# Kernel tuning notes

Hardware: AMD Instinct MI355X
Metric: run time of the kernel (lower is better)

Reference implementation:

```python
import jax, jax.numpy as jnp
import numpy as np

B, H, I = 64, 4096, 14336   # batch, hidden, expert intermediate
NLUT = 4096                 # 2**L_bits, L=12
W_SCALE = 0.02              # payload['W_scale'] (same for all three here)


def _rademacher(key, shape):
    return jnp.where(jax.random.bernoulli(key, 0.5, shape), 1.0, -1.0).astype(jnp.float32)


def setup_inputs() -> dict:
    key = jax.random.key(0)
    ks = jax.random.split(key, 14)
    inp = {
        "x": jax.random.normal(ks[0], (B, H), jnp.float32),
        "lut_gate": jax.random.normal(ks[1], (NLUT,), jnp.float32) * 0.05,
        "lut_up": jax.random.normal(ks[2], (NLUT,), jnp.float32) * 0.05,
        "lut_down": jax.random.normal(ks[3], (NLUT,), jnp.float32) * 0.05,
        "gate_walks": jax.random.randint(ks[4], (I, H), 0, NLUT, jnp.int32),
        "up_walks": jax.random.randint(ks[5], (I, H), 0, NLUT, jnp.int32),
        "down_walks": jax.random.randint(ks[6], (H, I), 0, NLUT, jnp.int32),
        "gate_sign_l": _rademacher(ks[7], (I,)),
        "gate_sign_r": _rademacher(ks[8], (H,)),
        "up_sign_l": _rademacher(ks[9], (I,)),
        "up_sign_r": _rademacher(ks[10], (H,)),
        "down_sign_l": _rademacher(ks[11], (H,)),
        "down_sign_r": _rademacher(ks[12], (I,)),
    }
    return inp


def _dequant(lut, walks, sign_l, sign_r):
    # trellis-walk LUT gather per weight element, then row/col signs and scalar scale
    # walks: (out, in) int codes; lut: (NLUT,)
    return (lut[walks] * sign_l[:, None] * sign_r[None, :]) * W_SCALE


def reference(x, lut_gate, lut_up, lut_down,
              gate_walks, up_walks, down_walks,
              gate_sign_l, gate_sign_r, up_sign_l, up_sign_r,
              down_sign_l, down_sign_r):
    W_gate = _dequant(lut_gate, gate_walks, gate_sign_l, gate_sign_r)  # (I, H)
    W_up = _dequant(lut_up, up_walks, up_sign_l, up_sign_r)            # (I, H)
    W_down = _dequant(lut_down, down_walks, down_sign_l, down_sign_r)  # (H, I)
    gate_out = jax.nn.silu(x @ W_gate.T)   # (B, I)
    up_out = x @ W_up.T                    # (B, I)
    hidden = gate_out * up_out
    return hidden @ W_down.T               # (B, H)
```

## Files before the change

kernel.cpp:

```cpp
#include <hip/hip_runtime.h>
#include <hip/hip_bf16.h>

#define HD   4096
#define ID   14336
#define NB   64
#define NLUTN 4096
#define DKS  8

typedef __attribute__((ext_vector_type(8))) short short8;
typedef __attribute__((ext_vector_type(4))) float f32x4;

__device__ __forceinline__ unsigned short f2bf(float f) {
  __hip_bfloat16 h = __float2bfloat16(f);
  return __builtin_bit_cast(unsigned short, h);
}

__device__ __forceinline__ void gll16(const int* g, void* l) {
  __builtin_amdgcn_global_load_lds(
      (const __attribute__((address_space(1))) int*)g,
      (__attribute__((address_space(3))) int*)l, 16, 0, 0);
}

__global__ __launch_bounds__(256) void prep_kernel(
    const float* __restrict__ x, const float* __restrict__ gsr,
    const float* __restrict__ usr,
    unsigned short* __restrict__ xgB, unsigned short* __restrict__ xuB)
{
  int u = blockIdx.x * 256 + threadIdx.x;
  int b = u & 63, k8 = u >> 6;
  const float* xp = x + (size_t)b * HD + k8 * 8;
  float4 x0 = ((const float4*)xp)[0];
  float4 x1 = ((const float4*)xp)[1];
  const float* gp = gsr + k8 * 8;
  const float* up = usr + k8 * 8;
  float4 g0 = ((const float4*)gp)[0], g1 = ((const float4*)gp)[1];
  float4 u0 = ((const float4*)up)[0], u1 = ((const float4*)up)[1];
  ushort4 og0 = make_ushort4(f2bf(x0.x*g0.x), f2bf(x0.y*g0.y), f2bf(x0.z*g0.z), f2bf(x0.w*g0.w));
  ushort4 og1 = make_ushort4(f2bf(x1.x*g1.x), f2bf(x1.y*g1.y), f2bf(x1.z*g1.z), f2bf(x1.w*g1.w));
  ushort4 ou0 = make_ushort4(f2bf(x0.x*u0.x), f2bf(x0.y*u0.y), f2bf(x0.z*u0.z), f2bf(x0.w*u0.w));
  ushort4 ou1 = make_ushort4(f2bf(x1.x*u1.x), f2bf(x1.y*u1.y), f2bf(x1.z*u1.z), f2bf(x1.w*u1.w));
  ((ushort4*)(xgB + (size_t)u*8))[0] = og0;
  ((ushort4*)(xgB + (size_t)u*8))[1] = og1;
  ((ushort4*)(xuB + (size_t)u*8))[0] = ou0;
  ((ushort4*)(xuB + (size_t)u*8))[1] = ou1;
}

__global__ __launch_bounds__(128, 2) void gate_up_kernel(
    const int* __restrict__ gw, const int* __restrict__ uw,
    const float* __restrict__ lutg_f, const float* __restrict__ lutu_f,
    const unsigned short* __restrict__ xgB, const unsigned short* __restrict__ xuB,
    const float* __restrict__ gsl, const float* __restrict__ usl,
    const float* __restrict__ dsr,
    unsigned short* __restrict__ hidB)
{
  __shared__ unsigned short lutg[NLUTN];
  __shared__ unsigned short lutu[NLUTN];
  __shared__ __align__(16) int cbuf[2][2][2][2][512];
  __shared__ f32x4 red[16][64];

  const int tid  = threadIdx.x;
  const int lane = tid & 63;
  const int w    = tid >> 6;

  for (int i = tid; i < NLUTN/4; i += 128) {
    float4 g = ((const float4*)lutg_f)[i];
    float4 u = ((const float4*)lutu_f)[i];
    ((ushort4*)lutg)[i] = make_ushort4(f2bf(g.x), f2bf(g.y), f2bf(g.z), f2bf(g.w));
    ((ushort4*)lutu)[i] = make_ushort4(f2bf(u.x), f2bf(u.y), f2bf(u.z), f2bf(u.w));
  }
  __syncthreads();

  const int col  = lane & 15;
  const int quad = lane >> 4;
  const int m0   = blockIdx.x * 32;
  const int r8   = lane >> 3;
  const int j    = lane & 7;
  const int jx   = (j ^ r8) << 2;
  const int xsw  = (col & 7) << 4;

  const int kbeg = w * (HD/2);
  const int NIT  = (HD/2) / 32;

  const int* gsrc[2][2];
  const int* usrc[2][2];
  #pragma unroll
  for (int s = 0; s < 2; ++s)
    #pragma unroll
    for (int h = 0; h < 2; ++h) {
      int row = m0 + s*16 + h*8 + r8;
      gsrc[s][h] = gw + (size_t)row * HD + jx;
      usrc[s][h] = uw + (size_t)row * HD + jx;
    }

  const f32x4 z = {0.f, 0.f, 0.f, 0.f};
  f32x4 accg[2][4] = {{z,z,z,z},{z,z,z,z}};
  f32x4 accu[2][4] = {{z,z,z,z},{z,z,z,z}};

  #pragma unroll
  for (int s = 0; s < 2; ++s)
    #pragma unroll
    for (int h = 0; h < 2; ++h) {
      gll16(gsrc[s][h] + kbeg, (char*)&cbuf[w][0][0][s][0] + h*1024);
      gll16(usrc[s][h] + kbeg, (char*)&cbuf[w][0][1][s][0] + h*1024);
    }

  int p = 0;
  for (int it = 0; it < NIT; ++it) {
    const int k0 = kbeg + it*32;
    asm volatile("s_waitcnt vmcnt(0)" ::: "memory");
    __builtin_amdgcn_sched_barrier(0);

    short8 afg[2], afu[2];
    #pragma unroll
    for (int s = 0; s < 2; ++s) {
      const char* cg = (const char*)&cbuf[w][p][0][s][0];
      const char* cu = (const char*)&cbuf[w][p][1][s][0];
      int4 ga = *(const int4*)(cg + col*128 + (((quad<<5) + 0 ) ^ xsw));
      int4 gb = *(const int4*)(cg + col*128 + (((quad<<5) + 16) ^ xsw));
      int4 ua = *(const int4*)(cu + col*128 + (((quad<<5) + 0 ) ^ xsw));
      int4 ub = *(const int4*)(cu + col*128 + (((quad<<5) + 16) ^ xsw));
      afg[s][0] = (short)lutg[ga.x]; afg[s][1] = (short)lutg[ga.y];
      afg[s][2] = (short)lutg[ga.z]; afg[s][3] = (short)lutg[ga.w];
      afg[s][4] = (short)lutg[gb.x]; afg[s][5] = (short)lutg[gb.y];
      afg[s][6] = (short)lutg[gb.z]; afg[s][7] = (short)lutg[gb.w];
      afu[s][0] = (short)lutu[ua.x]; afu[s][1] = (short)lutu[ua.y];
      afu[s][2] = (short)lutu[ua.z]; afu[s][3] = (short)lutu[ua.w];
      afu[s][4] = (short)lutu[ub.x]; afu[s][5] = (short)lutu[ub.y];
      afu[s][6] = (short)lutu[ub.z]; afu[s][7] = (short)lutu[ub.w];
    }

    const size_t xoff = ((size_t)((k0 >> 3) + quad) * 64 + col) * 8;
    short8 bgv[4], buv[4];
    #pragma unroll
    for (int t = 0; t < 4; ++t) {
      bgv[t] = __builtin_bit_cast(short8, *(const int4*)(xgB + xoff + t*128));
      buv[t] = __builtin_bit_cast(short8, *(const int4*)(xuB + xoff + t*128));
    }
    __builtin_amdgcn_sched_barrier(0);

    const int kn = (it == NIT-1) ? kbeg : k0 + 32;
    #pragma unroll
    for (int s = 0; s < 2; ++s)
      #pragma unroll
      for (int h = 0; h < 2; ++h) {
        gll16(gsrc[s][h] + kn, (char*)&cbuf[w][p^1][0][s][0] + h*1024);
        gll16(usrc[s][h] + kn, (char*)&cbuf[w][p^1][1][s][0] + h*1024);
      }

    #pragma unroll
    for (int t = 0; t < 4; ++t)
      #pragma unroll
      for (int s = 0; s < 2; ++s) {
        accg[s][t] = __builtin_amdgcn_mfma_f32_16x16x32_bf16(afg[s], bgv[t], accg[s][t], 0, 0, 0);
        accu[s][t] = __builtin_amdgcn_mfma_f32_16x16x32_bf16(afu[s], buv[t], accu[s][t], 0, 0, 0);
      }
    p ^= 1;
  }

  if (w == 1) {
    #pragma unroll
    for (int s = 0; s < 2; ++s)
      #pragma unroll
      for (int t = 0; t < 4; ++t) {
        red[(s*4+t)*2+0][lane] = accg[s][t];
        red[(s*4+t)*2+1][lane] = accu[s][t];
      }
  }
  __syncthreads();
  if (w == 0) {
    #pragma unroll
    for (int s = 0; s < 2; ++s) {
      const int mrow = m0 + s*16 + quad*4;
      float sg[4], su[4], sd[4];
      #pragma unroll
      for (int r = 0; r < 4; ++r) {
        sg[r] = 0.02f * gsl[mrow + r];
        su[r] = 0.02f * usl[mrow + r];
        sd[r] = dsr[mrow + r];
      }
      #pragma unroll
      for (int t = 0; t < 4; ++t) {
        f32x4 ag = accg[s][t] + red[(s*4+t)*2+0][lane];
        f32x4 au = accu[s][t] + red[(s*4+t)*2+1][lane];
        int b = t*16 + col;
        float g0 = ag[0]*sg[0], u0 = au[0]*su[0];
        float g1 = ag[1]*sg[1], u1 = au[1]*su[1];
        float g2 = ag[2]*sg[2], u2 = au[2]*su[2];
        float g3 = ag[3]*sg[3], u3 = au[3]*su[3];
        ushort4 hv;
        hv.x = f2bf((g0 / (1.f + __expf(-g0))) * u0 * sd[0]);
        hv.y = f2bf((g1 / (1.f + __expf(-g1))) * u1 * sd[1]);
        hv.z = f2bf((g2 / (1.f + __expf(-g2))) * u2 * sd[2]);
        hv.w = f2bf((g3 / (1.f + __expf(-g3))) * u3 * sd[3]);
        *(ushort4*)(hidB + ((size_t)((mrow >> 3)*64 + b))*8 + (quad & 1)*4) = hv;
      }
    }
  }
}

__global__ __launch_bounds__(128, 2) void down_kernel(
    const int* __restrict__ dw, const float* __restrict__ lutd_f,
    const unsigned short* __restrict__ hidB,
    const float* __restrict__ dsl,
    float* __restrict__ out)
{
  __shared__ unsigned short lutd[NLUTN];
  __shared__ __align__(16) int cbuf[2][2][2][512];
  __shared__ f32x4 red[8][64];

  const int tid  = threadIdx.x;
  const int lane = tid & 63;
  const int w    = tid >> 6;

  for (int i = tid; i < NLUTN/4; i += 128) {
    float4 d = ((const float4*)lutd_f)[i];
    ((ushort4*)lutd)[i] = make_ushort4(f2bf(d.x), f2bf(d.y), f2bf(d.z), f2bf(d.w));
  }
  __syncthreads();

  const int col  = lane & 15;
  const int quad = lane >> 4;
  const int m0   = blockIdx.x * 32;
  const int r8   = lane >> 3;
  const int j    = lane & 7;
  const int jx   = (j ^ r8) << 2;
  const int xsw  = (col & 7) << 4;

  const int kbeg = blockIdx.y * (ID/DKS) + w * (ID/DKS/2);
  const int NIT  = (ID/DKS/2) / 32;

  const int* dsrc[2][2];
  #pragma unroll
  for (int s = 0; s < 2; ++s)
    #pragma unroll
    for (int h = 0; h < 2; ++h) {
      int row = m0 + s*16 + h*8 + r8;
      dsrc[s][h] = dw + (size_t)row * ID + jx;
    }

  const f32x4 z = {0.f, 0.f, 0.f, 0.f};
  f32x4 acc[2][4] = {{z,z,z,z},{z,z,z,z}};

  #pragma unroll
  for (int s = 0; s < 2; ++s)
    #pragma unroll
    for (int h = 0; h < 2; ++h)
      gll16(dsrc[s][h] + kbeg, (char*)&cbuf[w][0][s][0] + h*1024);

  int p = 0;
  for (int it = 0; it < NIT; ++it) {
    const int k0 = kbeg + it*32;
    asm volatile("s_waitcnt vmcnt(0)" ::: "memory");
    __builtin_amdgcn_sched_barrier(0);

    short8 af[2];
    #pragma unroll
    for (int s = 0; s < 2; ++s) {
      const char* cd = (const char*)&cbuf[w][p][s][0];
      int4 da = *(const int4*)(cd + col*128 + (((quad<<5) + 0 ) ^ xsw));
      int4 db = *(const int4*)(cd + col*128 + (((quad<<5) + 16) ^ xsw));
      af[s][0] = (short)lutd[da.x]; af[s][1] = (short)lutd[da.y];
      af[s][2] = (short)lutd[da.z]; af[s][3] = (short)lutd[da.w];
      af[s][4] = (short)lutd[db.x]; af[s][5] = (short)lutd[db.y];
      af[s][6] = (short)lutd[db.z]; af[s][7] = (short)lutd[db.w];
    }

    const size_t xoff = ((size_t)((k0 >> 3) + quad) * 64 + col) * 8;
    short8 bh[4];
    #pragma unroll
    for (int t = 0; t < 4; ++t)
      bh[t] = __builtin_bit_cast(short8, *(const int4*)(hidB + xoff + t*128));
    __builtin_amdgcn_sched_barrier(0);

    const int kn = (it == NIT-1) ? kbeg : k0 + 32;
    #pragma unroll
    for (int s = 0; s < 2; ++s)
      #pragma unroll
      for (int h = 0; h < 2; ++h)
        gll16(dsrc[s][h] + kn, (char*)&cbuf[w][p^1][s][0] + h*1024);

    #pragma unroll
    for (int t = 0; t < 4; ++t)
      #pragma unroll
      for (int s = 0; s < 2; ++s)
        acc[s][t] = __builtin_amdgcn_mfma_f32_16x16x32_bf16(af[s], bh[t], acc[s][t], 0, 0, 0);
    p ^= 1;
  }

  if (w == 1) {
    #pragma unroll
    for (int s = 0; s < 2; ++s)
      #pragma unroll
      for (int t = 0; t < 4; ++t)
        red[s*4+t][lane] = acc[s][t];
  }
  __syncthreads();
  if (w == 0) {
    #pragma unroll
    for (int s = 0; s < 2; ++s) {
      const int mrow = m0 + s*16 + quad*4;
      float sc[4];
      #pragma unroll
      for (int r = 0; r < 4; ++r) sc[r] = 0.02f * dsl[mrow + r];
      #pragma unroll
      for (int t = 0; t < 4; ++t) {
        f32x4 a = acc[s][t] + red[s*4+t][lane];
        int b = t*16 + col;
        #pragma unroll
        for (int r = 0; r < 4; ++r)
          atomicAdd(&out[(size_t)b * HD + mrow + r], a[r] * sc[r]);
      }
    }
  }
}

extern "C" void kernel_launch(void* const* d_in, const int* in_sizes, int n_in,
                              void* d_out, int out_size, void* d_ws, size_t ws_size,
                              hipStream_t stream) {
  const float* x    = (const float*)d_in[0];
  const float* lutg = (const float*)d_in[1];
  const float* lutu = (const float*)d_in[2];
  const float* lutd = (const float*)d_in[3];
  const int*   gw   = (const int*)d_in[4];
  const int*   uw   = (const int*)d_in[5];
  const int*   dw   = (const int*)d_in[6];
  const float* gsl  = (const float*)d_in[7];
  const float* gsr  = (const float*)d_in[8];
  const float* usl  = (const float*)d_in[9];
  const float* usr  = (const float*)d_in[10];
  const float* dsl  = (const float*)d_in[11];
  const float* dsr  = (const float*)d_in[12];
  float* out = (float*)d_out;

  unsigned short* xgB  = (unsigned short*)d_ws;
  unsigned short* xuB  = xgB + (size_t)NB * HD;
  unsigned short* hidB = xuB + (size_t)NB * HD;

  hipMemsetAsync(d_out, 0, (size_t)NB * HD * sizeof(float), stream);
  prep_kernel<<<(NB*HD/8 + 255)/256, 256, 0, stream>>>(x, gsr, usr, xgB, xuB);
  gate_up_kernel<<<ID/32, 128, 0, stream>>>(gw, uw, lutg, lutu, xgB, xuB,
                                            gsl, usl, dsr, hidB);
  down_kernel<<<dim3(HD/32, DKS), 128, 0, stream>>>(dw, lutd, hidB, dsl, out);
}
```

Before: 655.5 us.

## Split gate/up across waves, triple-buffer code loads with partial vmcnt waits

The gate_up kernel now assigns the gate projection to one wave and the up projection to the other, each over the full K range, and halves the rows per block so the grid doubles. Both kernels switch from a double buffer drained with vmcnt(0) to a three-stage LDS ring with vmcnt(6), and they prefetch the activation fragments one iteration ahead, so loads stay in flight during the LUT gathers and MFMAs. The down kernel gives each wave its own 16 output rows and drops the cross-wave LDS reduction, issuing atomics directly. In exchange, each wave has fewer MFMAs per LUT gather and loads less weight data per iteration, and the hand-tuned wait count has to match the number of outstanding loads exactly.

```diff
diff --git a/kernel.cpp b/kernel.cpp
--- a/kernel.cpp
+++ b/kernel.cpp
@@ -55,8 +55,8 @@
 {
   __shared__ unsigned short lutg[NLUTN];
   __shared__ unsigned short lutu[NLUTN];
-  __shared__ __align__(16) int cbuf[2][2][2][2][512];
-  __shared__ f32x4 red[16][64];
+  __shared__ __align__(16) int cbuf[2][3][512];
+  __shared__ f32x4 red[4][64];
 
   const int tid  = threadIdx.x;
   const int lane = tid & 63;
@@ -70,130 +70,101 @@
   }
   __syncthreads();
 
+  const unsigned short* lut = w ? lutu : lutg;
+  const int* cw = w ? uw : gw;
+  const unsigned short* xB = w ? xuB : xgB;
+
   const int col  = lane & 15;
   const int quad = lane >> 4;
-  const int m0   = blockIdx.x * 32;
+  const int m0   = blockIdx.x * 16;
   const int r8   = lane >> 3;
   const int j    = lane & 7;
   const int jx   = (j ^ r8) << 2;
   const int xsw  = (col & 7) << 4;
 
-  const int kbeg = w * (HD/2);
-  const int NIT  = (HD/2) / 32;
-
-  const int* gsrc[2][2];
-  const int* usrc[2][2];
-  #pragma unroll
-  for (int s = 0; s < 2; ++s)
-    #pragma unroll
-    for (int h = 0; h < 2; ++h) {
-      int row = m0 + s*16 + h*8 + r8;
-      gsrc[s][h] = gw + (size_t)row * HD + jx;
-      usrc[s][h] = uw + (size_t)row * HD + jx;
-    }
+  const int* src0 = cw + (size_t)(m0 + r8) * HD + jx;
+  const int* src1 = cw + (size_t)(m0 + 8 + r8) * HD + jx;
+
+  int* b0 = &cbuf[w][0][0];
+  int* b1 = &cbuf[w][1][0];
+  int* b2 = &cbuf[w][2][0];
 
   const f32x4 z = {0.f, 0.f, 0.f, 0.f};
-  f32x4 accg[2][4] = {{z,z,z,z},{z,z,z,z}};
-  f32x4 accu[2][4] = {{z,z,z,z},{z,z,z,z}};
-
-  #pragma unroll
-  for (int s = 0; s < 2; ++s)
-    #pragma unroll
-    for (int h = 0; h < 2; ++h) {
-      gll16(gsrc[s][h] + kbeg, (char*)&cbuf[w][0][0][s][0] + h*1024);
-      gll16(usrc[s][h] + kbeg, (char*)&cbuf[w][0][1][s][0] + h*1024);
-    }
-
-  int p = 0;
+  f32x4 acc[4] = {z, z, z, z};
+
+  gll16(src0 + 0, b0); gll16(src1 + 0, (char*)b0 + 1024);
+  short8 xv[4];
+  {
+    size_t xo = ((size_t)quad * 64 + col) * 8;
+    #pragma unroll
+    for (int t = 0; t < 4; ++t)
+      xv[t] = __builtin_bit_cast(short8, *(const int4*)(xB + xo + t*128));
+  }
+  gll16(src0 + 32, b1); gll16(src1 + 32, (char*)b1 + 1024);
+
+  const int NIT = HD / 32;
   for (int it = 0; it < NIT; ++it) {
-    const int k0 = kbeg + it*32;
-    asm volatile("s_waitcnt vmcnt(0)" ::: "memory");
+    asm volatile("s_waitcnt vmcnt(6)" ::: "memory");
     __builtin_amdgcn_sched_barrier(0);
 
-    short8 afg[2], afu[2];
-    #pragma unroll
-    for (int s = 0; s < 2; ++s) {
-      const char* cg = (const char*)&cbuf[w][p][0][s][0];
-      const char* cu = (const char*)&cbuf[w][p][1][s][0];
-      int4 ga = *(const int4*)(cg + col*128 + (((quad<<5) + 0 ) ^ xsw));
-      int4 gb = *(const int4*)(cg + col*128 + (((quad<<5) + 16) ^ xsw));
-      int4 ua = *(const int4*)(cu + col*128 + (((quad<<5) + 0 ) ^ xsw));
-      int4 ub = *(const int4*)(cu + col*128 + (((quad<<5) + 16) ^ xsw));
-      afg[s][0] = (short)lutg[ga.x]; afg[s][1] = (short)lutg[ga.y];
-      afg[s][2] = (short)lutg[ga.z]; afg[s][3] = (short)lutg[ga.w];
-      afg[s][4] = (short)lutg[gb.x]; afg[s][5] = (short)lutg[gb.y];
-      afg[s][6] = (short)lutg[gb.z]; afg[s][7] = (short)lutg[gb.w];
-      afu[s][0] = (short)lutu[ua.x]; afu[s][1] = (short)lutu[ua.y];
-      afu[s][2] = (short)lutu[ua.z]; afu[s][3] = (short)lutu[ua.w];
-      afu[s][4] = (short)lutu[ub.x]; afu[s][5] = (short)lutu[ub.y];
-      afu[s][6] = (short)lutu[ub.z]; afu[s][7] = (short)lutu[ub.w];
-    }
-
-    const size_t xoff = ((size_t)((k0 >> 3) + quad) * 64 + col) * 8;
-    short8 bgv[4], buv[4];
-    #pragma unroll
-    for (int t = 0; t < 4; ++t) {
-      bgv[t] = __builtin_bit_cast(short8, *(const int4*)(xgB + xoff + t*128));
-      buv[t] = __builtin_bit_cast(short8, *(const int4*)(xuB + xoff + t*128));
-    }
-    __builtin_amdgcn_sched_barrier(0);
-
-    const int kn = (it == NIT-1) ? kbeg : k0 + 32;
-    #pragma unroll
-    for (int s = 0; s < 2; ++s)
+    const char* cg = (const char*)b0;
+    int4 ca = *(const int4*)(cg + col*128 + (((quad<<5) + 0 ) ^ xsw));
+    int4 cb = *(const int4*)(cg + col*128 + (((quad<<5) + 16) ^ xsw));
+    short8 af;
+    af[0] = (short)lut[ca.x]; af[1] = (short)lut[ca.y];
+    af[2] = (short)lut[ca.z]; af[3] = (short)lut[ca.w];
+    af[4] = (short)lut[cb.x]; af[5] = (short)lut[cb.y];
+    af[6] = (short)lut[cb.z]; af[7] = (short)lut[cb.w];
+
+    const int kx = (it+1 < NIT) ? (it+1)*32 : 0;
+    short8 xn[4];
+    {
+      size_t xo = ((size_t)((kx >> 3) + quad) * 64 + col) * 8;
       #pragma unroll
-      for (int h = 0; h < 2; ++h) {
-        gll16(gsrc[s][h] + kn, (char*)&cbuf[w][p^1][0][s][0] + h*1024);
-        gll16(usrc[s][h] + kn, (char*)&cbuf[w][p^1][1][s][0] + h*1024);
-      }
-
-    #pragma unroll
-    for (int t = 0; t < 4; ++t)
-      #pragma unroll
-      for (int s = 0; s < 2; ++s) {
-        accg[s][t] = __builtin_amdgcn_mfma_f32_16x16x32_bf16(afg[s], bgv[t], accg[s][t], 0, 0, 0);
-        accu[s][t] = __builtin_amdgcn_mfma_f32_16x16x32_bf16(afu[s], buv[t], accu[s][t], 0, 0, 0);
-      }
-    p ^= 1;
+      for (int t = 0; t < 4; ++t)
+        xn[t] = __builtin_bit_cast(short8, *(const int4*)(xB + xo + t*128));
+    }
+
+    const int ks = (it+2 < NIT) ? (it+2)*32 : 0;
+    gll16(src0 + ks, b2); gll16(src1 + ks, (char*)b2 + 1024);
+
+    #pragma unroll
+    for (int t = 0; t < 4; ++t)
+      acc[t] = __builtin_amdgcn_mfma_f32_16x16x32_bf16(af, xv[t], acc[t], 0, 0, 0);
+
+    #pragma unroll
+    for (int t = 0; t < 4; ++t) xv[t] = xn[t];
+    int* tmp = b0; b0 = b1; b1 = b2; b2 = tmp;
   }
 
   if (w == 1) {
     #pragma unroll
-    for (int s = 0; s < 2; ++s)
-      #pragma unroll
-      for (int t = 0; t < 4; ++t) {
-        red[(s*4+t)*2+0][lane] = accg[s][t];
-        red[(s*4+t)*2+1][lane] = accu[s][t];
-      }
+    for (int t = 0; t < 4; ++t) red[t][lane] = acc[t];
   }
   __syncthreads();
   if (w == 0) {
-    #pragma unroll
-    for (int s = 0; s < 2; ++s) {
-      const int mrow = m0 + s*16 + quad*4;
-      float sg[4], su[4], sd[4];
-      #pragma unroll
-      for (int r = 0; r < 4; ++r) {
-        sg[r] = 0.02f * gsl[mrow + r];
-        su[r] = 0.02f * usl[mrow + r];
-        sd[r] = dsr[mrow + r];
-      }
-      #pragma unroll
-      for (int t = 0; t < 4; ++t) {
-        f32x4 ag = accg[s][t] + red[(s*4+t)*2+0][lane];
-        f32x4 au = accu[s][t] + red[(s*4+t)*2+1][lane];
-        int b = t*16 + col;
-        float g0 = ag[0]*sg[0], u0 = au[0]*su[0];
-        float g1 = ag[1]*sg[1], u1 = au[1]*su[1];
-        float g2 = ag[2]*sg[2], u2 = au[2]*su[2];
-        float g3 = ag[3]*sg[3], u3 = au[3]*su[3];
-        ushort4 hv;
-        hv.x = f2bf((g0 / (1.f + __expf(-g0))) * u0 * sd[0]);
-        hv.y = f2bf((g1 / (1.f + __expf(-g1))) * u1 * sd[1]);
-        hv.z = f2bf((g2 / (1.f + __expf(-g2))) * u2 * sd[2]);
-        hv.w = f2bf((g3 / (1.f + __expf(-g3))) * u3 * sd[3]);
-        *(ushort4*)(hidB + ((size_t)((mrow >> 3)*64 + b))*8 + (quad & 1)*4) = hv;
-      }
+    const int mrow = m0 + quad * 4;
+    float sg[4], su[4], sd[4];
+    #pragma unroll
+    for (int r = 0; r < 4; ++r) {
+      sg[r] = 0.02f * gsl[mrow + r];
+      su[r] = 0.02f * usl[mrow + r];
+      sd[r] = dsr[mrow + r];
+    }
+    #pragma unroll
+    for (int t = 0; t < 4; ++t) {
+      f32x4 au = red[t][lane];
+      int b = t*16 + col;
+      float g0 = acc[t][0]*sg[0], u0 = au[0]*su[0];
+      float g1 = acc[t][1]*sg[1], u1 = au[1]*su[1];
+      float g2 = acc[t][2]*sg[2], u2 = au[2]*su[2];
+      float g3 = acc[t][3]*sg[3], u3 = au[3]*su[3];
+      ushort4 hv;
+      hv.x = f2bf((g0 / (1.f + __expf(-g0))) * u0 * sd[0]);
+      hv.y = f2bf((g1 / (1.f + __expf(-g1))) * u1 * sd[1]);
+      hv.z = f2bf((g2 / (1.f + __expf(-g2))) * u2 * sd[2]);
+      hv.w = f2bf((g3 / (1.f + __expf(-g3))) * u3 * sd[3]);
+      *(ushort4*)(hidB + ((size_t)((mrow >> 3)*64 + b))*8 + (quad & 1)*4) = hv;
     }
   }
 }
@@ -205,8 +176,7 @@
     float* __restrict__ out)
 {
   __shared__ unsigned short lutd[NLUTN];
-  __shared__ __align__(16) int cbuf[2][2][2][512];
-  __shared__ f32x4 red[8][64];
+  __shared__ __align__(16) int cbuf[2][3][512];
 
   const int tid  = threadIdx.x;
   const int lane = tid & 63;
@@ -220,97 +190,79 @@
 
   const int col  = lane & 15;
   const int quad = lane >> 4;
-  const int m0   = blockIdx.x * 32;
+  const int m0   = blockIdx.x * 32 + w * 16;
   const int r8   = lane >> 3;
   const int j    = lane & 7;
   const int jx   = (j ^ r8) << 2;
   const int xsw  = (col & 7) << 4;
 
-  const int kbeg = blockIdx.y * (ID/DKS) + w * (ID/DKS/2);
-  const int NIT  = (ID/DKS/2) / 32;
-
-  const int* dsrc[2][2];
-  #pragma unroll
-  for (int s = 0; s < 2; ++s)
-    #pragma unroll
-    for (int h = 0; h < 2; ++h) {
-      int row = m0 + s*16 + h*8 + r8;
-      dsrc[s][h] = dw + (size_t)row * ID + jx;
-    }
+  const int kbeg = blockIdx.y * (ID / DKS);
+  const int NIT  = (ID / DKS) / 32;
+
+  const int* src0 = dw + (size_t)(m0 + r8) * ID + kbeg + jx;
+  const int* src1 = dw + (size_t)(m0 + 8 + r8) * ID + kbeg + jx;
+
+  int* b0 = &cbuf[w][0][0];
+  int* b1 = &cbuf[w][1][0];
+  int* b2 = &cbuf[w][2][0];
 
   const f32x4 z = {0.f, 0.f, 0.f, 0.f};
-  f32x4 acc[2][4] = {{z,z,z,z},{z,z,z,z}};
-
-  #pragma unroll
-  for (int s = 0; s < 2; ++s)
-    #pragma unroll
-    for (int h = 0; h < 2; ++h)
-      gll16(dsrc[s][h] + kbeg, (char*)&cbuf[w][0][s][0] + h*1024);
-
-  int p = 0;
+  f32x4 acc[4] = {z, z, z, z};
+
+  gll16(src0 + 0, b0); gll16(src1 + 0, (char*)b0 + 1024);
+  short8 xv[4];
+  {
+    size_t xo = ((size_t)((kbeg >> 3) + quad) * 64 + col) * 8;
+    #pragma unroll
+    for (int t = 0; t < 4; ++t)
+      xv[t] = __builtin_bit_cast(short8, *(const int4*)(hidB + xo + t*128));
+  }
+  gll16(src0 + 32, b1); gll16(src1 + 32, (char*)b1 + 1024);
+
   for (int it = 0; it < NIT; ++it) {
-    const int k0 = kbeg + it*32;
-    asm volatile("s_waitcnt vmcnt(0)" ::: "memory");
+    asm volatile("s_waitcnt vmcnt(6)" ::: "memory");
     __builtin_amdgcn_sched_barrier(0);
 
-    short8 af[2];
-    #pragma unroll
-    for (int s = 0; s < 2; ++s) {
-      const char* cd = (const char*)&cbuf[w][p][s][0];
-      int4 da = *(const int4*)(cd + col*128 + (((quad<<5) + 0 ) ^ xsw));
-      int4 db = *(const int4*)(cd + col*128 + (((quad<<5) + 16) ^ xsw));
-      af[s][0] = (short)lutd[da.x]; af[s][1] = (short)lutd[da.y];
-      af[s][2] = (short)lutd[da.z]; af[s][3] = (short)lutd[da.w];
-      af[s][4] = (short)lutd[db.x]; af[s][5] = (short)lutd[db.y];
-      af[s][6] = (short)lutd[db.z]; af[s][7] = (short)lutd[db.w];
-    }
-
-    const size_t xoff = ((size_t)((k0 >> 3) + quad) * 64 + col) * 8;
-    short8 bh[4];
-    #pragma unroll
-    for (int t = 0; t < 4; ++t)
-      bh[t] = __builtin_bit_cast(short8, *(const int4*)(hidB + xoff + t*128));
-    __builtin_amdgcn_sched_barrier(0);
-
-    const int kn = (it == NIT-1) ? kbeg : k0 + 32;
-    #pragma unroll
-    for (int s = 0; s < 2; ++s)
-      #pragma unroll
-      for (int h = 0; h < 2; ++h)
-        gll16(dsrc[s][h] + kn, (char*)&cbuf[w][p^1][s][0] + h*1024);
-
-    #pragma unroll
-    for (int t = 0; t < 4; ++t)
-      #pragma unroll
-      for (int s = 0; s < 2; ++s)
-        acc[s][t] = __builtin_amdgcn_mfma_f32_16x16x32_bf16(af[s], bh[t], acc[s][t], 0, 0, 0);
-    p ^= 1;
-  }
-
-  if (w == 1) {
-    #pragma unroll
-    for (int s = 0; s < 2; ++s)
+    const char* cd = (const char*)b0;
+    int4 ca = *(const int4*)(cd + col*128 + (((quad<<5) + 0 ) ^ xsw));
+    int4 cb = *(const int4*)(cd + col*128 + (((quad<<5) + 16) ^ xsw));
+    short8 af;
+    af[0] = (short)lutd[ca.x]; af[1] = (short)lutd[ca.y];
+    af[2] = (short)lutd[ca.z]; af[3] = (short)lutd[ca.w];
+    af[4] = (short)lutd[cb.x]; af[5] = (short)lutd[cb.y];
+    af[6] = (short)lutd[cb.z]; af[7] = (short)lutd[cb.w];
+
+    const int kx = (it+1 < NIT) ? kbeg + (it+1)*32 : kbeg;
+    short8 xn[4];
+    {
+      size_t xo = ((size_t)((kx >> 3) + quad) * 64 + col) * 8;
       #pragma unroll
       for (int t = 0; t < 4; ++t)
-        red[s*4+t][lane] = acc[s][t];
-  }
-  __syncthreads();
-  if (w == 0) {
-    #pragma unroll
-    for (int s = 0; s < 2; ++s) {
-      const int mrow = m0 + s*16 + quad*4;
-      float sc[4];
-      #pragma unroll
-      for (int r = 0; r < 4; ++r) sc[r] = 0.02f * dsl[mrow + r];
-      #pragma unroll
-      for (int t = 0; t < 4; ++t) {
-        f32x4 a = acc[s][t] + red[s*4+t][lane];
-        int b = t*16 + col;
-        #pragma unroll
-        for (int r = 0; r < 4; ++r)
-          atomicAdd(&out[(size_t)b * HD + mrow + r], a[r] * sc[r]);
-      }
-    }
+        xn[t] = __builtin_bit_cast(short8, *(const int4*)(hidB + xo + t*128));
+    }
+
+    const int ks = (it+2 < NIT) ? (it+2)*32 : 0;
+    gll16(src0 + ks, b2); gll16(src1 + ks, (char*)b2 + 1024);
+
+    #pragma unroll
+    for (int t = 0; t < 4; ++t)
+      acc[t] = __builtin_amdgcn_mfma_f32_16x16x32_bf16(af, xv[t], acc[t], 0, 0, 0);
+
+    #pragma unroll
+    for (int t = 0; t < 4; ++t) xv[t] = xn[t];
+    int* tmp = b0; b0 = b1; b1 = b2; b2 = tmp;
+  }
+
+  const int mrow = m0 + quad * 4;
+  float sc[4];
+  #pragma unroll
+  for (int r = 0; r < 4; ++r) sc[r] = 0.02f * dsl[mrow + r];
+  #pragma unroll
+  for (int t = 0; t < 4; ++t) {
+    int b = t*16 + col;
+    #pragma unroll
+    for (int r = 0; r < 4; ++r)
+      atomicAdd(&out[(size_t)b * HD + mrow + r], acc[t][r] * sc[r]);
   }
 }
 
@@ -338,7 +290,7 @@
 
   hipMemsetAsync(d_out, 0, (size_t)NB * HD * sizeof(float), stream);
   prep_kernel<<<(NB*HD/8 + 255)/256, 256, 0, stream>>>(x, gsr, usr, xgB, xuB);
-  gate_up_kernel<<<ID/32, 128, 0, stream>>>(gw, uw, lutg, lutu, xgB, xuB,
+  gate_up_kernel<<<ID/16, 128, 0, stream>>>(gw, uw, lutg, lutu, xgB, xuB,
                                             gsl, usl, dsr, hidB);
   down_kernel<<<dim3(HD/32, DKS), 128, 0, stream>>>(dw, lutd, hidB, dsl, out);
 }
```

Result: slower. 675.2 us (+3.0%).
